# Kernel optimization log

Measured on AMD Instinct MI355X. Metric: run time of the kernel, lower is better.

Reference implementation:

```python
import jax, jax.numpy as jnp
import numpy as np

B, S, H, D = 2, 2048, 2048, 256  # batch, seq, hidden, head_dim
NH, NKV = 8, 1                   # attention heads, kv heads
N_REP = NH // NKV
SCALING = D ** -0.5
ROPE_THETA = 10000.0
NEG_INF = -1e9


def rotate_half(x):
    x1, x2 = jnp.split(x, 2, axis=-1)
    return jnp.concatenate((-x2, x1), axis=-1)


def setup_inputs() -> dict:
    key = jax.random.key(0)
    ks = jax.random.split(key, 5)
    hidden_states = jax.random.normal(ks[0], (B, S, H), dtype=jnp.float32)
    # RoPE cos/sin per position, Gemma-style: inv_freq tiled over full head_dim
    inv_freq = 1.0 / (ROPE_THETA ** (np.arange(0, D, 2, dtype=np.float32) / D))  # [D/2]
    pos = np.arange(S, dtype=np.float32)
    freqs = np.outer(pos, inv_freq)                      # [S, D/2]
    emb = np.concatenate([freqs, freqs], axis=-1)        # [S, D]
    cos = jnp.broadcast_to(jnp.asarray(np.cos(emb)), (B, S, D))
    sin = jnp.broadcast_to(jnp.asarray(np.sin(emb)), (B, S, D))
    # additive causal mask [B, 1, S, S]
    causal = jnp.triu(jnp.full((S, S), NEG_INF, dtype=jnp.float32), k=1)
    attention_mask = jnp.broadcast_to(causal[None, None], (B, 1, S, S))
    scale = 0.02
    Wq = jax.random.normal(ks[1], (H, NH * D), dtype=jnp.float32) * scale
    Wk = jax.random.normal(ks[2], (H, NKV * D), dtype=jnp.float32) * scale
    Wv = jax.random.normal(ks[3], (H, NKV * D), dtype=jnp.float32) * scale
    Wo = jax.random.normal(ks[4], (NH * D, H), dtype=jnp.float32) * scale
    return {"hidden_states": hidden_states, "cos": cos, "sin": sin,
            "attention_mask": attention_mask, "Wq": Wq, "Wk": Wk, "Wv": Wv, "Wo": Wo}


def reference(hidden_states, cos, sin, attention_mask, Wq, Wk, Wv, Wo):
    # projections: [B,S,H] @ [H, nh*D] -> [B, nh, S, D]
    q = (hidden_states @ Wq).reshape(B, S, NH, D).transpose(0, 2, 1, 3)
    k = (hidden_states @ Wk).reshape(B, S, NKV, D).transpose(0, 2, 1, 3)
    v = (hidden_states @ Wv).reshape(B, S, NKV, D).transpose(0, 2, 1, 3)
    # RoPE (cos/sin broadcast over head dim via unsqueeze at axis 1)
    c = cos[:, None]  # [B,1,S,D]
    s = sin[:, None]
    q = q * c + rotate_half(q) * s
    k = k * c + rotate_half(k) * s
    # repeat_kv: [B, NKV, S, D] -> [B, NH, S, D]
    k = jnp.repeat(k, N_REP, axis=1)
    v = jnp.repeat(v, N_REP, axis=1)
    # eager attention
    attn_weights = jnp.einsum("bhqd,bhkd->bhqk", q, k) * SCALING
    attn_weights = attn_weights + attention_mask[:, :, :, :S]
    attn_weights = jax.nn.softmax(attn_weights.astype(jnp.float32), axis=-1).astype(q.dtype)
    attn_output = jnp.einsum("bhqk,bhkd->bhqd", attn_weights, v)
    attn_output = attn_output.transpose(0, 2, 1, 3).reshape(B, S, NH * D)
    attn_output = attn_output @ Wo
    return attn_output, attn_weights
```

## Files before the change

### kernel.cpp

```cpp
#include <hip/hip_runtime.h>
#include <hip/hip_bf16.h>

#define B_   2
#define S_   2048
#define H_   2048
#define D_   256
#define NH_  8

typedef unsigned short u16;
typedef __bf16 bf16x8 __attribute__((ext_vector_type(8)));
typedef float f32x4 __attribute__((ext_vector_type(4)));
typedef unsigned int uint4v __attribute__((ext_vector_type(4)));
typedef unsigned int uint2v __attribute__((ext_vector_type(2)));

#define AS1 __attribute__((address_space(1)))
#define AS3 __attribute__((address_space(3)))

__device__ __forceinline__ u16 f2bf(float x) {
  union { float f; unsigned u; } v; v.f = x;
  unsigned u = v.u;
  u += 0x7FFFu + ((u >> 16) & 1u);
  return (u16)(u >> 16);
}
__device__ __forceinline__ float bf2f(u16 x) {
  union { unsigned u; float f; } v; v.u = ((unsigned)x) << 16;
  return v.f;
}

__device__ __forceinline__ void gld_lds16(const u16* g, u16* l) {
  __builtin_amdgcn_global_load_lds((const AS1 unsigned int*)g,
                                   (AS3 unsigned int*)l, 16, 0, 0);
}

#define BM 128
#define BN 128
#define BK 32

enum GemmMode { MODE_PROJ = 0, MODE_QK = 1, MODE_PV = 2, MODE_WO = 3 };

template <int MODE>
__global__ __launch_bounds__(256)
void gemm_nt(const u16* __restrict__ A, const u16* __restrict__ Bb,
             void* __restrict__ Cp, float* __restrict__ rows,
             int K, int lda, int ldb, int ldc)
{
  const int bn = blockIdx.x, bm = blockIdx.y, bz = blockIdx.z;
  if (MODE == MODE_QK && bn > bm) return;
  const int m0 = bm * BM, n0 = bn * BN;

  const u16* Ap = A;
  const u16* Bp = Bb;
  float* Cf = (float*)Cp;
  u16*   Cu = (u16*)Cp;

  if constexpr (MODE == MODE_QK) {
    Ap   += (size_t)bz * S_ * D_;
    Bp   += (size_t)(bz >> 3) * S_ * D_;
    Cu   += (size_t)bz * S_ * S_;
    rows += (size_t)bz * S_;
  } else if constexpr (MODE == MODE_PV) {
    Ap   += (size_t)bz * S_ * S_;
    Bp   += (size_t)(bz >> 3) * D_ * S_;
    Cu   += (size_t)(bz >> 3) * S_ * (NH_ * D_) + (size_t)(bz & 7) * D_;
    rows += (size_t)bz * S_;
  }

  int Keff = K;
  if constexpr (MODE == MODE_PV) {
    int lim = (bm + 1) * BM;
    Keff = lim < K ? lim : K;
  }

  __shared__ __align__(16) u16 As[BM * BK];
  __shared__ __align__(16) u16 Bs[BN * BK];

  const int tid  = threadIdx.x;
  const int lane = tid & 63;
  const int quad = lane >> 4;
  const int l16  = lane & 15;
  const int wave = tid >> 6;
  const int wm   = (wave >> 1) << 6;
  const int wn   = (wave & 1) << 6;

  f32x4 acc[4][4] = {};

  for (int kt = 0; kt < Keff; kt += BK) {
    #pragma unroll
    for (int i = 0; i < 2; i++) {
      int c = tid + i * 256;
      gld_lds16(Ap + (size_t)(m0 + (c >> 2)) * lda + kt + (c & 3) * 8, &As[c * 8]);
    }
    #pragma unroll
    for (int i = 0; i < 2; i++) {
      int c = tid + i * 256;
      gld_lds16(Bp + (size_t)(n0 + (c >> 2)) * ldb + kt + (c & 3) * 8, &Bs[c * 8]);
    }
    __syncthreads();

    bf16x8 af[4], bfr[4];
    #pragma unroll
    for (int i = 0; i < 4; i++)
      af[i] = *(const bf16x8*)(&As[(wm + i * 16 + l16) * BK + quad * 8]);
    #pragma unroll
    for (int j = 0; j < 4; j++)
      bfr[j] = *(const bf16x8*)(&Bs[(wn + j * 16 + l16) * BK + quad * 8]);
    #pragma unroll
    for (int i = 0; i < 4; i++)
      #pragma unroll
      for (int j = 0; j < 4; j++)
        acc[i][j] = __builtin_amdgcn_mfma_f32_16x16x32_bf16(af[i], bfr[j], acc[i][j], 0, 0, 0);
    __syncthreads();
  }

  const float SCL2 = 0.0625f * 1.44269504088896340736f;
  #pragma unroll
  for (int i = 0; i < 4; i++) {
    #pragma unroll
    for (int r = 0; r < 4; r++) {
      const int m = m0 + wm + i * 16 + quad * 4 + r;
      if constexpr (MODE == MODE_QK) {
        float rs = 0.f;
        #pragma unroll
        for (int j = 0; j < 4; j++) {
          int n = n0 + wn + j * 16 + l16;
          float e = (n <= m) ? exp2f(acc[i][j][r] * SCL2) : 0.f;
          rs += e;
          Cu[(size_t)m * ldc + n] = f2bf(e);
        }
        #pragma unroll
        for (int o = 1; o < 16; o <<= 1) rs += __shfl_xor(rs, o, 64);
        if (l16 == 0) atomicAdd(&rows[m], rs);
      } else if constexpr (MODE == MODE_PV) {
        float inv = 1.0f / rows[m];
        #pragma unroll
        for (int j = 0; j < 4; j++) {
          int n = n0 + wn + j * 16 + l16;
          Cu[(size_t)m * ldc + n] = f2bf(acc[i][j][r] * inv);
        }
      } else if constexpr (MODE == MODE_WO) {
        #pragma unroll
        for (int j = 0; j < 4; j++) {
          int n = n0 + wn + j * 16 + l16;
          Cf[(size_t)m * ldc + n] = acc[i][j][r];
        }
      } else {
        #pragma unroll
        for (int j = 0; j < 4; j++) {
          int n = n0 + wn + j * 16 + l16;
          Cu[(size_t)m * ldc + n] = f2bf(acc[i][j][r]);
        }
      }
    }
  }
}

__global__ __launch_bounds__(256)
void convert_bf16_kernel(const float* __restrict__ src, u16* __restrict__ dst, int n4)
{
  int i = blockIdx.x * 256 + threadIdx.x;
  if (i >= n4) return;
  float4 f = ((const float4*)src)[i];
  uint2v p;
  p.x = (unsigned)f2bf(f.x) | ((unsigned)f2bf(f.y) << 16);
  p.y = (unsigned)f2bf(f.z) | ((unsigned)f2bf(f.w) << 16);
  ((uint2v*)dst)[i] = p;
}

__global__ __launch_bounds__(256)
void transpose_convert(const float* __restrict__ src, u16* __restrict__ dst, int K, int N)
{
  __shared__ float t[32][33];
  int n0 = blockIdx.x * 32, k0 = blockIdx.y * 32;
  int c = threadIdx.x & 31, r = threadIdx.x >> 5;
  #pragma unroll
  for (int rr = 0; rr < 32; rr += 8)
    t[r + rr][c] = src[(size_t)(k0 + r + rr) * N + n0 + c];
  __syncthreads();
  #pragma unroll
  for (int rr = 0; rr < 32; rr += 8)
    dst[(size_t)(n0 + r + rr) * K + k0 + c] = f2bf(t[c][r + rr]);
}

__global__ __launch_bounds__(256)
void transpose_v_kernel(const u16* __restrict__ v, u16* __restrict__ vt)
{
  __shared__ u16 t[32][34];
  int b = blockIdx.z;
  int d0 = blockIdx.x * 32, s0 = blockIdx.y * 32;
  int c = threadIdx.x & 31, r = threadIdx.x >> 5;
  #pragma unroll
  for (int rr = 0; rr < 32; rr += 8)
    t[r + rr][c] = v[(size_t)(b * S_ + s0 + r + rr) * 2560 + 2304 + d0 + c];
  __syncthreads();
  #pragma unroll
  for (int rr = 0; rr < 32; rr += 8)
    vt[(size_t)b * D_ * S_ + (size_t)(d0 + r + rr) * S_ + s0 + c] = t[c][r + rr];
}

__global__ __launch_bounds__(256)
void rope_q_kernel(const u16* __restrict__ qraw, const float* __restrict__ cosb,
                   const float* __restrict__ sinb, u16* __restrict__ qout)
{
  int idx = blockIdx.x;
  int h = idx & 7, bs = idx >> 3;
  int b = bs >> 11, s = bs & (S_ - 1);
  int d = threadIdx.x;
  size_t base = (size_t)bs * 2560 + (size_t)h * D_;
  float qv = bf2f(qraw[base + d]);
  float qp = bf2f(qraw[base + (d ^ 128)]);
  float c  = cosb[(size_t)bs * D_ + d];
  float sn = sinb[(size_t)bs * D_ + d];
  float rot = (d < 128) ? -qp : qp;
  qout[(((size_t)b * NH_ + h) * S_ + s) * D_ + d] = f2bf(qv * c + rot * sn);
}

__global__ __launch_bounds__(256)
void rope_k_kernel(const u16* __restrict__ kraw, const float* __restrict__ cosb,
                   const float* __restrict__ sinb, u16* __restrict__ kout)
{
  int bs = blockIdx.x;
  int d = threadIdx.x;
  size_t base = (size_t)bs * 2560 + 2048;
  float kv = bf2f(kraw[base + d]);
  float kp = bf2f(kraw[base + (d ^ 128)]);
  float c  = cosb[(size_t)bs * D_ + d];
  float sn = sinb[(size_t)bs * D_ + d];
  float rot = (d < 128) ? -kp : kp;
  kout[(size_t)bs * D_ + d] = f2bf(kv * c + rot * sn);
}

__global__ __launch_bounds__(256)
void normalize_p(const u16* __restrict__ E, const float* __restrict__ rows,
                 float* __restrict__ P)
{
  const int r = blockIdx.x;
  const int q = r & (S_ - 1);
  const u16* e = E + (size_t)r * S_;
  float* p = P + (size_t)r * S_;
  const float inv = 1.0f / rows[r];
  const int k0 = threadIdx.x * 8;

  float4 lo = {0.f, 0.f, 0.f, 0.f}, hi = {0.f, 0.f, 0.f, 0.f};
  if (k0 <= q) {
    uint4v u = *(const uint4v*)(e + k0);
    float v[8];
    v[0] = bf2f(u.x & 0xffff); v[1] = bf2f(u.x >> 16);
    v[2] = bf2f(u.y & 0xffff); v[3] = bf2f(u.y >> 16);
    v[4] = bf2f(u.z & 0xffff); v[5] = bf2f(u.z >> 16);
    v[6] = bf2f(u.w & 0xffff); v[7] = bf2f(u.w >> 16);
    lo.x = (k0 + 0 <= q) ? v[0] * inv : 0.f;
    lo.y = (k0 + 1 <= q) ? v[1] * inv : 0.f;
    lo.z = (k0 + 2 <= q) ? v[2] * inv : 0.f;
    lo.w = (k0 + 3 <= q) ? v[3] * inv : 0.f;
    hi.x = (k0 + 4 <= q) ? v[4] * inv : 0.f;
    hi.y = (k0 + 5 <= q) ? v[5] * inv : 0.f;
    hi.z = (k0 + 6 <= q) ? v[6] * inv : 0.f;
    hi.w = (k0 + 7 <= q) ? v[7] * inv : 0.f;
  }
  *(float4*)(p + k0)     = lo;
  *(float4*)(p + k0 + 4) = hi;
}

extern "C" void kernel_launch(void* const* d_in, const int* in_sizes, int n_in,
                              void* d_out, int out_size, void* d_ws, size_t ws_size,
                              hipStream_t stream)
{
  const float* X    = (const float*)d_in[0];
  const float* cosb = (const float*)d_in[1];
  const float* sinb = (const float*)d_in[2];
  const float* Wq   = (const float*)d_in[4];
  const float* Wk   = (const float*)d_in[5];
  const float* Wv   = (const float*)d_in[6];
  const float* Wo   = (const float*)d_in[7];

  float* outO = (float*)d_out;
  float* outP = outO + (size_t)B_ * S_ * H_;

  u16* ws     = (u16*)d_ws;
  u16* Xbf    = ws;
  u16* WT     = Xbf    + 8388608;
  u16* WoT    = WT     + 5242880;
  u16* QKVraw = WoT    + 4194304;
  u16* Qbf    = QKVraw + 10485760;
  u16* Kbf    = Qbf    + 8388608;
  u16* VT     = Kbf    + 1048576;
  u16* AObf   = VT     + 1048576;
  u16* Ebf    = AObf   + 8388608;
  float* Rows = (float*)(Ebf + 67108864);

  convert_bf16_kernel<<<8192, 256, 0, stream>>>(X, Xbf, 2097152);
  transpose_convert<<<dim3(64, 64), 256, 0, stream>>>(Wq, WT, 2048, 2048);
  transpose_convert<<<dim3(8, 64),  256, 0, stream>>>(Wk, WT + 2048 * 2048, 2048, 256);
  transpose_convert<<<dim3(8, 64),  256, 0, stream>>>(Wv, WT + 2304 * 2048, 2048, 256);
  transpose_convert<<<dim3(64, 64), 256, 0, stream>>>(Wo, WoT, 2048, 2048);
  gemm_nt<MODE_PROJ><<<dim3(20, 32, 1), 256, 0, stream>>>(
      Xbf, WT, QKVraw, nullptr, 2048, 2048, 2048, 2560);
  rope_q_kernel<<<32768, 256, 0, stream>>>(QKVraw, cosb, sinb, Qbf);
  rope_k_kernel<<<4096, 256, 0, stream>>>(QKVraw, cosb, sinb, Kbf);
  transpose_v_kernel<<<dim3(8, 64, 2), 256, 0, stream>>>(QKVraw, VT);
  hipMemsetAsync(Rows, 0, 32768 * sizeof(float), stream);
  gemm_nt<MODE_QK><<<dim3(16, 16, 16), 256, 0, stream>>>(
      Qbf, Kbf, Ebf, Rows, 256, 256, 256, 2048);
  normalize_p<<<32768, 256, 0, stream>>>(Ebf, Rows, outP);
  gemm_nt<MODE_PV><<<dim3(2, 16, 16), 256, 0, stream>>>(
      Ebf, VT, AObf, Rows, 2048, 2048, 2048, 2048);
  gemm_nt<MODE_WO><<<dim3(16, 32, 1), 256, 0, stream>>>(
      AObf, WoT, outO, nullptr, 2048, 2048, 2048, 2048);
}
```

Before: 706.4 us.

## Double GEMM K-tile, stage bf16 epilogue through LDS, merge prep kernels

Raises the GEMM K-tile from 32 to 64 so each barrier pair covers twice the MFMA work, and stages the bf16 output tile through padded shared memory so global stores become coalesced 16-byte writes. It also merges the weight/input conversion kernels into one launch, and the RoPE, V-transpose and row-sum zeroing into another, to cut launch count. Shared memory per block grows, which may lower occupancy, and the epilogue adds an extra barrier.

```diff
diff --git a/kernel.cpp b/kernel.cpp
--- a/kernel.cpp
+++ b/kernel.cpp
@@ -34,7 +34,8 @@
 
 #define BM 128
 #define BN 128
-#define BK 32
+#define BK 64
+#define CPAD 132
 
 enum GemmMode { MODE_PROJ = 0, MODE_QK = 1, MODE_PV = 2, MODE_WO = 3 };
 
@@ -71,8 +72,10 @@
     Keff = lim < K ? lim : K;
   }
 
-  __shared__ __align__(16) u16 As[BM * BK];
-  __shared__ __align__(16) u16 Bs[BN * BK];
+  __shared__ __align__(16) char smem[CPAD * BM * 2];
+  u16* sA = (u16*)smem;
+  u16* sB = sA + BM * BK;
+  u16* sC = (u16*)smem;
 
   const int tid  = threadIdx.x;
   const int lane = tid & 63;
@@ -86,38 +89,56 @@
 
   for (int kt = 0; kt < Keff; kt += BK) {
     #pragma unroll
-    for (int i = 0; i < 2; i++) {
+    for (int i = 0; i < 4; i++) {
       int c = tid + i * 256;
-      gld_lds16(Ap + (size_t)(m0 + (c >> 2)) * lda + kt + (c & 3) * 8, &As[c * 8]);
+      gld_lds16(Ap + (size_t)(m0 + (c >> 3)) * lda + kt + (c & 7) * 8, &sA[c * 8]);
     }
     #pragma unroll
-    for (int i = 0; i < 2; i++) {
+    for (int i = 0; i < 4; i++) {
       int c = tid + i * 256;
-      gld_lds16(Bp + (size_t)(n0 + (c >> 2)) * ldb + kt + (c & 3) * 8, &Bs[c * 8]);
+      gld_lds16(Bp + (size_t)(n0 + (c >> 3)) * ldb + kt + (c & 7) * 8, &sB[c * 8]);
     }
     __syncthreads();
 
-    bf16x8 af[4], bfr[4];
-    #pragma unroll
-    for (int i = 0; i < 4; i++)
-      af[i] = *(const bf16x8*)(&As[(wm + i * 16 + l16) * BK + quad * 8]);
-    #pragma unroll
-    for (int j = 0; j < 4; j++)
-      bfr[j] = *(const bf16x8*)(&Bs[(wn + j * 16 + l16) * BK + quad * 8]);
+    #pragma unroll
+    for (int ks = 0; ks < BK; ks += 32) {
+      bf16x8 af[4], bfr[4];
+      #pragma unroll
+      for (int i = 0; i < 4; i++)
+        af[i] = *(const bf16x8*)(&sA[(wm + i * 16 + l16) * BK + ks + quad * 8]);
+      #pragma unroll
+      for (int j = 0; j < 4; j++)
+        bfr[j] = *(const bf16x8*)(&sB[(wn + j * 16 + l16) * BK + ks + quad * 8]);
+      #pragma unroll
+      for (int i = 0; i < 4; i++)
+        #pragma unroll
+        for (int j = 0; j < 4; j++)
+          acc[i][j] = __builtin_amdgcn_mfma_f32_16x16x32_bf16(af[i], bfr[j], acc[i][j], 0, 0, 0);
+    }
+    __syncthreads();
+  }
+
+  const float SCL2 = 0.0625f * 1.44269504088896340736f;
+
+  if constexpr (MODE == MODE_WO) {
     #pragma unroll
     for (int i = 0; i < 4; i++)
       #pragma unroll
-      for (int j = 0; j < 4; j++)
-        acc[i][j] = __builtin_amdgcn_mfma_f32_16x16x32_bf16(af[i], bfr[j], acc[i][j], 0, 0, 0);
-    __syncthreads();
-  }
-
-  const float SCL2 = 0.0625f * 1.44269504088896340736f;
+      for (int r = 0; r < 4; r++) {
+        int m = m0 + wm + i * 16 + quad * 4 + r;
+        #pragma unroll
+        for (int j = 0; j < 4; j++)
+          Cf[(size_t)m * ldc + n0 + wn + j * 16 + l16] = acc[i][j][r];
+      }
+    return;
+  }
+
   #pragma unroll
   for (int i = 0; i < 4; i++) {
     #pragma unroll
     for (int r = 0; r < 4; r++) {
-      const int m = m0 + wm + i * 16 + quad * 4 + r;
+      const int mr = wm + i * 16 + quad * 4 + r;
+      const int m  = m0 + mr;
       if constexpr (MODE == MODE_QK) {
         float rs = 0.f;
         #pragma unroll
@@ -125,7 +146,7 @@
           int n = n0 + wn + j * 16 + l16;
           float e = (n <= m) ? exp2f(acc[i][j][r] * SCL2) : 0.f;
           rs += e;
-          Cu[(size_t)m * ldc + n] = f2bf(e);
+          sC[mr * CPAD + wn + j * 16 + l16] = f2bf(e);
         }
         #pragma unroll
         for (int o = 1; o < 16; o <<= 1) rs += __shfl_xor(rs, o, 64);
@@ -133,44 +154,31 @@
       } else if constexpr (MODE == MODE_PV) {
         float inv = 1.0f / rows[m];
         #pragma unroll
-        for (int j = 0; j < 4; j++) {
-          int n = n0 + wn + j * 16 + l16;
-          Cu[(size_t)m * ldc + n] = f2bf(acc[i][j][r] * inv);
-        }
-      } else if constexpr (MODE == MODE_WO) {
-        #pragma unroll
-        for (int j = 0; j < 4; j++) {
-          int n = n0 + wn + j * 16 + l16;
-          Cf[(size_t)m * ldc + n] = acc[i][j][r];
-        }
+        for (int j = 0; j < 4; j++)
+          sC[mr * CPAD + wn + j * 16 + l16] = f2bf(acc[i][j][r] * inv);
       } else {
         #pragma unroll
-        for (int j = 0; j < 4; j++) {
-          int n = n0 + wn + j * 16 + l16;
-          Cu[(size_t)m * ldc + n] = f2bf(acc[i][j][r]);
-        }
+        for (int j = 0; j < 4; j++)
+          sC[mr * CPAD + wn + j * 16 + l16] = f2bf(acc[i][j][r]);
       }
     }
   }
-}
-
-__global__ __launch_bounds__(256)
-void convert_bf16_kernel(const float* __restrict__ src, u16* __restrict__ dst, int n4)
-{
-  int i = blockIdx.x * 256 + threadIdx.x;
-  if (i >= n4) return;
-  float4 f = ((const float4*)src)[i];
-  uint2v p;
-  p.x = (unsigned)f2bf(f.x) | ((unsigned)f2bf(f.y) << 16);
-  p.y = (unsigned)f2bf(f.z) | ((unsigned)f2bf(f.w) << 16);
-  ((uint2v*)dst)[i] = p;
-}
-
-__global__ __launch_bounds__(256)
-void transpose_convert(const float* __restrict__ src, u16* __restrict__ dst, int K, int N)
+  __syncthreads();
+  #pragma unroll
+  for (int p = 0; p < 8; p++) {
+    int row = p * 16 + (tid >> 4);
+    int col = (tid & 15) * 8;
+    uint4v x = *(const uint4v*)(&sC[row * CPAD + col]);
+    *(uint4v*)(Cu + (size_t)(m0 + row) * ldc + n0 + col) = x;
+  }
+}
+
+__device__ __forceinline__ void tconv_tile(const float* __restrict__ src,
+                                           u16* __restrict__ dst,
+                                           int K, int N, int bx, int by)
 {
   __shared__ float t[32][33];
-  int n0 = blockIdx.x * 32, k0 = blockIdx.y * 32;
+  int n0 = bx * 32, k0 = by * 32;
   int c = threadIdx.x & 31, r = threadIdx.x >> 5;
   #pragma unroll
   for (int rr = 0; rr < 32; rr += 8)
@@ -182,51 +190,76 @@
 }
 
 __global__ __launch_bounds__(256)
-void transpose_v_kernel(const u16* __restrict__ v, u16* __restrict__ vt)
-{
-  __shared__ u16 t[32][34];
-  int b = blockIdx.z;
-  int d0 = blockIdx.x * 32, s0 = blockIdx.y * 32;
-  int c = threadIdx.x & 31, r = threadIdx.x >> 5;
-  #pragma unroll
-  for (int rr = 0; rr < 32; rr += 8)
-    t[r + rr][c] = v[(size_t)(b * S_ + s0 + r + rr) * 2560 + 2304 + d0 + c];
-  __syncthreads();
-  #pragma unroll
-  for (int rr = 0; rr < 32; rr += 8)
-    vt[(size_t)b * D_ * S_ + (size_t)(d0 + r + rr) * S_ + s0 + c] = t[c][r + rr];
+void prep_kernel(const float* __restrict__ X,
+                 const float* __restrict__ Wq, const float* __restrict__ Wk,
+                 const float* __restrict__ Wv, const float* __restrict__ Wo,
+                 u16* __restrict__ Xbf, u16* __restrict__ WT, u16* __restrict__ WoT)
+{
+  int b = blockIdx.x;
+  if (b < 8192) {
+    int i = b * 256 + threadIdx.x;
+    float4 f = ((const float4*)X)[i];
+    uint2v p;
+    p.x = (unsigned)f2bf(f.x) | ((unsigned)f2bf(f.y) << 16);
+    p.y = (unsigned)f2bf(f.z) | ((unsigned)f2bf(f.w) << 16);
+    ((uint2v*)Xbf)[i] = p;
+  } else if (b < 12288) {
+    int t = b - 8192;  tconv_tile(Wq, WT, 2048, 2048, t & 63, t >> 6);
+  } else if (b < 12800) {
+    int t = b - 12288; tconv_tile(Wk, WT + 2048 * 2048, 2048, 256, t & 7, t >> 3);
+  } else if (b < 13312) {
+    int t = b - 12800; tconv_tile(Wv, WT + 2304 * 2048, 2048, 256, t & 7, t >> 3);
+  } else {
+    int t = b - 13312; tconv_tile(Wo, WoT, 2048, 2048, t & 63, t >> 6);
+  }
 }
 
 __global__ __launch_bounds__(256)
-void rope_q_kernel(const u16* __restrict__ qraw, const float* __restrict__ cosb,
-                   const float* __restrict__ sinb, u16* __restrict__ qout)
-{
-  int idx = blockIdx.x;
-  int h = idx & 7, bs = idx >> 3;
-  int b = bs >> 11, s = bs & (S_ - 1);
-  int d = threadIdx.x;
-  size_t base = (size_t)bs * 2560 + (size_t)h * D_;
-  float qv = bf2f(qraw[base + d]);
-  float qp = bf2f(qraw[base + (d ^ 128)]);
-  float c  = cosb[(size_t)bs * D_ + d];
-  float sn = sinb[(size_t)bs * D_ + d];
-  float rot = (d < 128) ? -qp : qp;
-  qout[(((size_t)b * NH_ + h) * S_ + s) * D_ + d] = f2bf(qv * c + rot * sn);
-}
-
-__global__ __launch_bounds__(256)
-void rope_k_kernel(const u16* __restrict__ kraw, const float* __restrict__ cosb,
-                   const float* __restrict__ sinb, u16* __restrict__ kout)
-{
-  int bs = blockIdx.x;
-  int d = threadIdx.x;
-  size_t base = (size_t)bs * 2560 + 2048;
-  float kv = bf2f(kraw[base + d]);
-  float kp = bf2f(kraw[base + (d ^ 128)]);
-  float c  = cosb[(size_t)bs * D_ + d];
-  float sn = sinb[(size_t)bs * D_ + d];
-  float rot = (d < 128) ? -kp : kp;
-  kout[(size_t)bs * D_ + d] = f2bf(kv * c + rot * sn);
+void stage2_kernel(const u16* __restrict__ qkv, const float* __restrict__ cosb,
+                   const float* __restrict__ sinb, u16* __restrict__ qout,
+                   u16* __restrict__ kout, u16* __restrict__ vt,
+                   float* __restrict__ rows)
+{
+  int blk = blockIdx.x;
+  if (blk < 32768) {
+    int h = blk & 7, bs = blk >> 3;
+    int b = bs >> 11, s = bs & (S_ - 1);
+    int d = threadIdx.x;
+    size_t base = (size_t)bs * 2560 + (size_t)h * D_;
+    float qv = bf2f(qkv[base + d]);
+    float qp = bf2f(qkv[base + (d ^ 128)]);
+    float c  = cosb[(size_t)bs * D_ + d];
+    float sn = sinb[(size_t)bs * D_ + d];
+    float rot = (d < 128) ? -qp : qp;
+    qout[(((size_t)b * NH_ + h) * S_ + s) * D_ + d] = f2bf(qv * c + rot * sn);
+  } else if (blk < 36864) {
+    int bs = blk - 32768;
+    int d = threadIdx.x;
+    size_t base = (size_t)bs * 2560 + 2048;
+    float kv = bf2f(qkv[base + d]);
+    float kp = bf2f(qkv[base + (d ^ 128)]);
+    float c  = cosb[(size_t)bs * D_ + d];
+    float sn = sinb[(size_t)bs * D_ + d];
+    float rot = (d < 128) ? -kp : kp;
+    kout[(size_t)bs * D_ + d] = f2bf(kv * c + rot * sn);
+  } else if (blk < 37888) {
+    __shared__ u16 t[32][34];
+    int g = blk - 36864;
+    int b = g >> 9, rem = g & 511;
+    int d0 = (rem & 7) * 32, s0 = (rem >> 3) * 32;
+    int c = threadIdx.x & 31, r = threadIdx.x >> 5;
+    #pragma unroll
+    for (int rr = 0; rr < 32; rr += 8)
+      t[r + rr][c] = qkv[(size_t)(b * S_ + s0 + r + rr) * 2560 + 2304 + d0 + c];
+    __syncthreads();
+    #pragma unroll
+    for (int rr = 0; rr < 32; rr += 8)
+      vt[(size_t)b * D_ * S_ + (size_t)(d0 + r + rr) * S_ + s0 + c] = t[c][r + rr];
+  } else {
+    int g = blk - 37888;
+    float4 z = {0.f, 0.f, 0.f, 0.f};
+    ((float4*)rows)[g * 256 + threadIdx.x] = z;
+  }
 }
 
 __global__ __launch_bounds__(256)
@@ -288,17 +321,10 @@
   u16* Ebf    = AObf   + 8388608;
   float* Rows = (float*)(Ebf + 67108864);
 
-  convert_bf16_kernel<<<8192, 256, 0, stream>>>(X, Xbf, 2097152);
-  transpose_convert<<<dim3(64, 64), 256, 0, stream>>>(Wq, WT, 2048, 2048);
-  transpose_convert<<<dim3(8, 64),  256, 0, stream>>>(Wk, WT + 2048 * 2048, 2048, 256);
-  transpose_convert<<<dim3(8, 64),  256, 0, stream>>>(Wv, WT + 2304 * 2048, 2048, 256);
-  transpose_convert<<<dim3(64, 64), 256, 0, stream>>>(Wo, WoT, 2048, 2048);
+  prep_kernel<<<17408, 256, 0, stream>>>(X, Wq, Wk, Wv, Wo, Xbf, WT, WoT);
   gemm_nt<MODE_PROJ><<<dim3(20, 32, 1), 256, 0, stream>>>(
       Xbf, WT, QKVraw, nullptr, 2048, 2048, 2048, 2560);
-  rope_q_kernel<<<32768, 256, 0, stream>>>(QKVraw, cosb, sinb, Qbf);
-  rope_k_kernel<<<4096, 256, 0, stream>>>(QKVraw, cosb, sinb, Kbf);
-  transpose_v_kernel<<<dim3(8, 64, 2), 256, 0, stream>>>(QKVraw, VT);
-  hipMemsetAsync(Rows, 0, 32768 * sizeof(float), stream);
+  stage2_kernel<<<37920, 256, 0, stream>>>(QKVraw, cosb, sinb, Qbf, Kbf, VT, Rows);
   gemm_nt<MODE_QK><<<dim3(16, 16, 16), 256, 0, stream>>>(
       Qbf, Kbf, Ebf, Rows, 256, 256, 256, 2048);
   normalize_p<<<32768, 256, 0, stream>>>(Ebf, Rows, outP);
```

Result: slower. 741.6 us (+5.0%).
